# Kernel tuning notes

Measured on AMD Instinct MI355X. Metric: run time of the kernel, lower is better.

## Reference

```python
import jax, jax.numpy as jnp
import numpy as np

Q_LAYERS = 2

def _cnot(s, c, t):
    # s: [N,2,2,2,2]; wire w lives on axis w+1. Here t = c+1 always.
    s0 = jnp.take(s, 0, axis=c + 1)          # control=0 slice (axis removed)
    s1 = jnp.take(s, 1, axis=c + 1)          # control=1 slice
    t_ax = t + 1 - (1 if t > c else 0)       # target axis after removal
    s1 = jnp.flip(s1, axis=t_ax)             # X on target
    return jnp.stack([s0, s1], axis=c + 1)

def _ry(s, w, theta):
    a = w + 1
    co, si = jnp.cos(theta / 2), jnp.sin(theta / 2)
    s0 = jnp.take(s, 0, axis=a)
    s1 = jnp.take(s, 1, axis=a)
    return jnp.stack([co * s0 - si * s1, si * s0 + co * s1], axis=a)

def _quantum_features(x2d):
    # x2d: [B,28,28] -> per 2x2 patch angles [p00,p01,p10,p11]
    B = x2d.shape[0]
    p = x2d.reshape(B, 14, 2, 14, 2).transpose(0, 1, 3, 2, 4).reshape(-1, 4)  # [N,4]
    half = 0.5 * p
    c_, s_ = jnp.cos(half), jnp.sin(half)
    # RY(a_i)|0> product state, real amplitudes throughout (RY/CNOT only)
    state = (jnp.stack([c_[:, 0], s_[:, 0]], -1)[:, :, None, None, None]
             * jnp.stack([c_[:, 1], s_[:, 1]], -1)[:, None, :, None, None]
             * jnp.stack([c_[:, 2], s_[:, 2]], -1)[:, None, None, :, None]
             * jnp.stack([c_[:, 3], s_[:, 3]], -1)[:, None, None, None, :])
    qpi4 = jnp.asarray(np.pi / 4, dtype=state.dtype)
    for _ in range(Q_LAYERS):
        for w in range(3):
            state = _cnot(state, w, w + 1)
        state = _ry(state, 3, qpi4)
    probs = state * state
    z = jnp.stack([jnp.take(probs, 0, axis=w + 1).sum((1, 2, 3))
                   - jnp.take(probs, 1, axis=w + 1).sum((1, 2, 3))
                   for w in range(4)], axis=-1)      # [N,4]
    return z.reshape(B, 14 * 14 * 4)

def setup_inputs() -> dict:
    key = jax.random.key(0)
    ks = jax.random.split(key, 5)
    B = 8192
    return {
        'x': jax.random.normal(ks[0], (B, 1, 28, 28), dtype=jnp.float32),
        'conv_w': jax.random.normal(ks[1], (4, 1, 2, 2), dtype=jnp.float32) * 0.5,
        'conv_b': jax.random.normal(ks[2], (4,), dtype=jnp.float32) * 0.1,
        'fc_w': jax.random.normal(ks[3], (10, 1568), dtype=jnp.float32) * 0.02,
        'fc_b': jax.random.normal(ks[4], (10,), dtype=jnp.float32) * 0.02,
    }

def reference(x, conv_w, conv_b, fc_w, fc_b):
    B = x.shape[0]
    conv = jax.lax.conv_general_dilated(
        x, conv_w, window_strides=(2, 2), padding='VALID',
        dimension_numbers=('NCHW', 'OIHW', 'NCHW')) + conv_b[None, :, None, None]
    conv_flat = conv.reshape(B, -1)                   # [B, 4*14*14]
    q_feat = _quantum_features(x[:, 0])               # [B, 4*14*14]
    fused = jnp.concatenate([conv_flat, q_feat], axis=1)
    logits = fused @ fc_w.T + fc_b
    return jax.nn.log_softmax(logits, axis=-1)
```

## Files before the change

### kernel.cpp

```cpp
#include <hip/hip_runtime.h>


typedef _Float16 f16x8 __attribute__((ext_vector_type(8)));
typedef float    f32x4 __attribute__((ext_vector_type(4)));

__global__ __launch_bounds__(512, 4) void quanv_mfma(
    const float* __restrict__ x,
    const float* __restrict__ conv_w,
    const float* __restrict__ conv_b,
    const float* __restrict__ fc_w,
    const float* __restrict__ fc_b,
    float* __restrict__ out,
    int B)
{
    __shared__ float red[8][16][16];

    const int tid  = threadIdx.x;
    const int wid  = tid >> 6;
    const int lane = tid & 63;
    const int l15  = lane & 15;
    const int slot = lane >> 4;
    const int b0   = blockIdx.x * 16;

    float cw[16], cb[4];
#pragma unroll
    for (int i = 0; i < 16; ++i) cw[i] = conv_w[i];
#pragma unroll
    for (int i = 0; i < 4; ++i) cb[i] = conv_b[i];

    const int   o   = l15;
    const int   oc  = (o < 10) ? o : 9;
    const float msk = (o < 10) ? 1.f : 0.f;
    const float* wr = fc_w + oc * 1568;

    int img = b0 + l15;
    if (img >= B) img = B - 1;
    const float* xi = x + (size_t)img * 784;

    f32x4 acc = {0.f, 0.f, 0.f, 0.f};

    const int g0 = (wid * 49) >> 3;
    const int g1 = ((wid + 1) * 49) >> 3;

    for (int g = g0; g < g1; ++g) {
        const int p   = (g << 2) + slot;
        const int pi  = p / 14;
        const int pj  = p - pi * 14;
        const int off = pi * 56 + pj * 2;

        const float2 r0 = *reinterpret_cast<const float2*>(xi + off);
        const float2 r1 = *reinterpret_cast<const float2*>(xi + off + 28);
        const float x00 = r0.x, x01 = r0.y, x10 = r1.x, x11 = r1.y;

        const float ft0 = fmaf(x00, cw[0],  fmaf(x01, cw[1],  fmaf(x10, cw[2],  fmaf(x11, cw[3],  cb[0]))));
        const float ft1 = fmaf(x00, cw[4],  fmaf(x01, cw[5],  fmaf(x10, cw[6],  fmaf(x11, cw[7],  cb[1]))));
        const float ft2 = fmaf(x00, cw[8],  fmaf(x01, cw[9],  fmaf(x10, cw[10], fmaf(x11, cw[11], cb[2]))));
        const float ft3 = fmaf(x00, cw[12], fmaf(x01, cw[13], fmaf(x10, cw[14], fmaf(x11, cw[15], cb[3]))));

        const float c0 = __cosf(x00);
        const float c1 = __cosf(x01);
        const float c2 = __cosf(x10);
        const float s3 = __sinf(x11);
        const float c3 = __cosf(x11);
        const float t  = c0 * c2;
        const float u  = c1 * c3;
        const float z3 = 0.5f * ((u - s3) - t * (u + s3));

        f16x8 a;
        a[0] = (_Float16)ft0; a[1] = (_Float16)ft1;
        a[2] = (_Float16)ft2; a[3] = (_Float16)ft3;
        a[4] = (_Float16)c0;  a[5] = (_Float16)c1;
        a[6] = (_Float16)t;   a[7] = (_Float16)z3;

        const float  w0 = wr[p]       * msk;
        const float  w1 = wr[196 + p] * msk;
        const float  w2 = wr[392 + p] * msk;
        const float  w3 = wr[588 + p] * msk;
        const float4 wq = *reinterpret_cast<const float4*>(wr + 784 + p * 4);

        f16x8 b;
        b[0] = (_Float16)w0;          b[1] = (_Float16)w1;
        b[2] = (_Float16)w2;          b[3] = (_Float16)w3;
        b[4] = (_Float16)(wq.x * msk); b[5] = (_Float16)(wq.y * msk);
        b[6] = (_Float16)(wq.z * msk); b[7] = (_Float16)(wq.w * msk);

        acc = __builtin_amdgcn_mfma_f32_16x16x32_f16(a, b, acc, 0, 0, 0);
    }

#pragma unroll
    for (int r = 0; r < 4; ++r)
        red[wid][slot * 4 + r][l15] = acc[r];
    __syncthreads();

    if (tid < 256) {
        const int row = tid >> 4, col = tid & 15;
        float s = 0.f;
#pragma unroll
        for (int w = 0; w < 8; ++w) s += red[w][row][col];
        red[0][row][col] = s;
    }
    __syncthreads();

    if (tid < 16) {
        const int im = tid;
        if (b0 + im < B) {
            float lg[10];
#pragma unroll
            for (int j = 0; j < 10; ++j) lg[j] = red[0][im][j] + fc_b[j];
            float mx = lg[0];
#pragma unroll
            for (int j = 1; j < 10; ++j) mx = fmaxf(mx, lg[j]);
            float se = 0.f;
#pragma unroll
            for (int j = 0; j < 10; ++j) se += __expf(lg[j] - mx);
            const float lse = __logf(se) + mx;
            float* op = out + (size_t)(b0 + im) * 10;
#pragma unroll
            for (int j = 0; j < 10; ++j) op[j] = lg[j] - lse;
        }
    }
}

extern "C" void kernel_launch(void* const* d_in, const int* in_sizes, int n_in,
                              void* d_out, int out_size, void* d_ws, size_t ws_size,
                              hipStream_t stream) {
    const float* x      = (const float*)d_in[0];
    const float* conv_w = (const float*)d_in[1];
    const float* conv_b = (const float*)d_in[2];
    const float* fc_w   = (const float*)d_in[3];
    const float* fc_b   = (const float*)d_in[4];
    float* out = (float*)d_out;

    const int B = in_sizes[0] / 784;
    const int blocks = (B + 15) / 16;
    quanv_mfma<<<blocks, 512, 0, stream>>>(x, conv_w, conv_b, fc_w, fc_b, out, B);
}
```

Measured before the change: 20.66 us.

## Stage images in LDS with coalesced loads and preload weights before the loop

The 16 images of a block are copied into padded shared memory with coalesced float4 loads. Previously each lane did strided float2 gathers straight from global memory. All fc weight fragments are loaded and packed to f16 up front, the patch loop is interleaved across waves and fully unrolled, and f16 packing now uses cvt_pkrtz. This adds about 50KB of LDS per block, which may limit occupancy below the launch-bounds target. It also drops the clamp for a partial last block, so reads can go out of bounds when B is not a multiple of 16.

```diff
diff --git a/kernel.cpp b/kernel.cpp
--- a/kernel.cpp
+++ b/kernel.cpp
@@ -3,6 +3,9 @@
 
 typedef _Float16 f16x8 __attribute__((ext_vector_type(8)));
 typedef float    f32x4 __attribute__((ext_vector_type(4)));
+typedef unsigned int u32x4 __attribute__((ext_vector_type(4)));
+
+#define XSTRIDE 788
 
 __global__ __launch_bounds__(512, 4) void quanv_mfma(
     const float* __restrict__ x,
@@ -13,6 +16,7 @@
     float* __restrict__ out,
     int B)
 {
+    __shared__ __align__(16) float xl[16 * XSTRIDE];
     __shared__ float red[8][16][16];
 
     const int tid  = threadIdx.x;
@@ -22,69 +26,90 @@
     const int slot = lane >> 4;
     const int b0   = blockIdx.x * 16;
 
+    const int   o   = l15;
+    const int   oc  = (o < 10) ? o : 9;
+    const float msk = (o < 10) ? 1.f : 0.f;
+    const float* wr = fc_w + oc * 1568;
+
+    f16x8 bw[7];
+#pragma unroll
+    for (int j = 0; j < 7; ++j) {
+        const int g = wid + (j << 3);
+        if (g < 49) {
+            const int p = (g << 2) + slot;
+            const float w0 = wr[p]       * msk;
+            const float w1 = wr[196 + p] * msk;
+            const float w2 = wr[392 + p] * msk;
+            const float w3 = wr[588 + p] * msk;
+            const float4 wq = *reinterpret_cast<const float4*>(wr + 784 + p * 4);
+            u32x4 wu;
+            wu[0] = __builtin_bit_cast(unsigned int, __builtin_amdgcn_cvt_pkrtz(w0, w1));
+            wu[1] = __builtin_bit_cast(unsigned int, __builtin_amdgcn_cvt_pkrtz(w2, w3));
+            wu[2] = __builtin_bit_cast(unsigned int, __builtin_amdgcn_cvt_pkrtz(wq.x * msk, wq.y * msk));
+            wu[3] = __builtin_bit_cast(unsigned int, __builtin_amdgcn_cvt_pkrtz(wq.z * msk, wq.w * msk));
+            bw[j] = __builtin_bit_cast(f16x8, wu);
+        } else {
+            u32x4 z = {0u, 0u, 0u, 0u};
+            bw[j] = __builtin_bit_cast(f16x8, z);
+        }
+    }
+
     float cw[16], cb[4];
 #pragma unroll
     for (int i = 0; i < 16; ++i) cw[i] = conv_w[i];
 #pragma unroll
     for (int i = 0; i < 4; ++i) cb[i] = conv_b[i];
 
-    const int   o   = l15;
-    const int   oc  = (o < 10) ? o : 9;
-    const float msk = (o < 10) ? 1.f : 0.f;
-    const float* wr = fc_w + oc * 1568;
+    {
+        const float* xg = x + (size_t)b0 * 784;
+        for (int i = tid; i < 3136; i += 512) {
+            const float4 v = *reinterpret_cast<const float4*>(xg + 4 * i);
+            const int img = i / 196;
+            const int w   = (i - img * 196) * 4;
+            *reinterpret_cast<float4*>(&xl[img * XSTRIDE + w]) = v;
+        }
+    }
+    __syncthreads();
 
-    int img = b0 + l15;
-    if (img >= B) img = B - 1;
-    const float* xi = x + (size_t)img * 784;
-
+    const float* xim = &xl[l15 * XSTRIDE];
     f32x4 acc = {0.f, 0.f, 0.f, 0.f};
 
-    const int g0 = (wid * 49) >> 3;
-    const int g1 = ((wid + 1) * 49) >> 3;
+#pragma unroll
+    for (int j = 0; j < 7; ++j) {
+        const int g = wid + (j << 3);
+        if (g < 49) {
+            const int p   = (g << 2) + slot;
+            const int pi  = p / 14;
+            const int pj  = p - pi * 14;
+            const int off = pi * 56 + pj * 2;
 
-    for (int g = g0; g < g1; ++g) {
-        const int p   = (g << 2) + slot;
-        const int pi  = p / 14;
-        const int pj  = p - pi * 14;
-        const int off = pi * 56 + pj * 2;
+            const float2 r0 = *reinterpret_cast<const float2*>(xim + off);
+            const float2 r1 = *reinterpret_cast<const float2*>(xim + off + 28);
+            const float x00 = r0.x, x01 = r0.y, x10 = r1.x, x11 = r1.y;
 
-        const float2 r0 = *reinterpret_cast<const float2*>(xi + off);
-        const float2 r1 = *reinterpret_cast<const float2*>(xi + off + 28);
-        const float x00 = r0.x, x01 = r0.y, x10 = r1.x, x11 = r1.y;
+            const float ft0 = fmaf(x00, cw[0],  fmaf(x01, cw[1],  fmaf(x10, cw[2],  fmaf(x11, cw[3],  cb[0]))));
+            const float ft1 = fmaf(x00, cw[4],  fmaf(x01, cw[5],  fmaf(x10, cw[6],  fmaf(x11, cw[7],  cb[1]))));
+            const float ft2 = fmaf(x00, cw[8],  fmaf(x01, cw[9],  fmaf(x10, cw[10], fmaf(x11, cw[11], cb[2]))));
+            const float ft3 = fmaf(x00, cw[12], fmaf(x01, cw[13], fmaf(x10, cw[14], fmaf(x11, cw[15], cb[3]))));
 
-        const float ft0 = fmaf(x00, cw[0],  fmaf(x01, cw[1],  fmaf(x10, cw[2],  fmaf(x11, cw[3],  cb[0]))));
-        const float ft1 = fmaf(x00, cw[4],  fmaf(x01, cw[5],  fmaf(x10, cw[6],  fmaf(x11, cw[7],  cb[1]))));
-        const float ft2 = fmaf(x00, cw[8],  fmaf(x01, cw[9],  fmaf(x10, cw[10], fmaf(x11, cw[11], cb[2]))));
-        const float ft3 = fmaf(x00, cw[12], fmaf(x01, cw[13], fmaf(x10, cw[14], fmaf(x11, cw[15], cb[3]))));
+            const float c0 = __cosf(x00);
+            const float c1 = __cosf(x01);
+            const float c2 = __cosf(x10);
+            const float s3 = __sinf(x11);
+            const float c3 = __cosf(x11);
+            const float t  = c0 * c2;
+            const float u  = c1 * c3;
+            const float z3 = 0.5f * ((u - s3) - t * (u + s3));
 
-        const float c0 = __cosf(x00);
-        const float c1 = __cosf(x01);
-        const float c2 = __cosf(x10);
-        const float s3 = __sinf(x11);
-        const float c3 = __cosf(x11);
-        const float t  = c0 * c2;
-        const float u  = c1 * c3;
-        const float z3 = 0.5f * ((u - s3) - t * (u + s3));
+            u32x4 au;
+            au[0] = __builtin_bit_cast(unsigned int, __builtin_amdgcn_cvt_pkrtz(ft0, ft1));
+            au[1] = __builtin_bit_cast(unsigned int, __builtin_amdgcn_cvt_pkrtz(ft2, ft3));
+            au[2] = __builtin_bit_cast(unsigned int, __builtin_amdgcn_cvt_pkrtz(c0, c1));
+            au[3] = __builtin_bit_cast(unsigned int, __builtin_amdgcn_cvt_pkrtz(t, z3));
+            const f16x8 a = __builtin_bit_cast(f16x8, au);
 
-        f16x8 a;
-        a[0] = (_Float16)ft0; a[1] = (_Float16)ft1;
-        a[2] = (_Float16)ft2; a[3] = (_Float16)ft3;
-        a[4] = (_Float16)c0;  a[5] = (_Float16)c1;
-        a[6] = (_Float16)t;   a[7] = (_Float16)z3;
-
-        const float  w0 = wr[p]       * msk;
-        const float  w1 = wr[196 + p] * msk;
-        const float  w2 = wr[392 + p] * msk;
-        const float  w3 = wr[588 + p] * msk;
-        const float4 wq = *reinterpret_cast<const float4*>(wr + 784 + p * 4);
-
-        f16x8 b;
-        b[0] = (_Float16)w0;          b[1] = (_Float16)w1;
-        b[2] = (_Float16)w2;          b[3] = (_Float16)w3;
-        b[4] = (_Float16)(wq.x * msk); b[5] = (_Float16)(wq.y * msk);
-        b[6] = (_Float16)(wq.z * msk); b[7] = (_Float16)(wq.w * msk);
-
-        acc = __builtin_amdgcn_mfma_f32_16x16x32_f16(a, b, acc, 0, 0, 0);
+            acc = __builtin_amdgcn_mfma_f32_16x16x32_f16(a, bw[j], acc, 0, 0, 0);
+        }
     }
 
 #pragma unroll
```

After: 21.23 us. 2.8% more time.
